# Kernel tuning notes

Measured on AMD Instinct MI355X. Metric: run time of the kernel, lower is better.

Reference implementation:

```python
import jax, jax.numpy as jnp
import numpy as np

K = 32                      # nsample (neighbors)
NPTS = [4096, 2048, 1024]   # npts // downsample_ratios [1,2,4]
CH = [(6, 64, 64), (134, 128, 128), (262, 256, 256)]  # (c_in_edge, c_mid, c_out) per EdgeConv
OUT_CH = 128
EPS = 1e-5


def setup_inputs():
    key = jax.random.key(0)
    ks = iter(jax.random.split(key, 64))
    d = {"pcd": jax.random.normal(next(ks), (8, 4096, 3), dtype=jnp.float32)}
    for li, (cin, cmid, cout) in enumerate(CH, start=1):
        d[f"W{li}a"] = jax.random.normal(next(ks), (cmid, cin), dtype=jnp.float32) * 0.05
        d[f"b{li}a"] = jax.random.normal(next(ks), (cmid,), dtype=jnp.float32) * 0.01
        d[f"g{li}a"] = jnp.ones((cmid,), dtype=jnp.float32)
        d[f"be{li}a"] = jnp.zeros((cmid,), dtype=jnp.float32)
        d[f"W{li}b"] = jax.random.normal(next(ks), (cout, cmid), dtype=jnp.float32) * 0.05
        d[f"b{li}b"] = jax.random.normal(next(ks), (cout,), dtype=jnp.float32) * 0.01
        d[f"g{li}b"] = jnp.ones((cout,), dtype=jnp.float32)
        d[f"be{li}b"] = jnp.zeros((cout,), dtype=jnp.float32)
    d["fcW"] = jax.random.normal(next(ks), (OUT_CH, CH[-1][2]), dtype=jnp.float32) * 0.05
    d["fcb"] = jnp.zeros((OUT_CH,), dtype=jnp.float32)
    return d


def _knn_idx(q, p, k):
    # q: [B,m,3] queries, p: [B,n,3] points -> [B,m,k] nearest-neighbor indices
    d = (jnp.sum(q * q, -1)[:, :, None] + jnp.sum(p * p, -1)[:, None, :]
         - 2.0 * jnp.einsum('bmd,bnd->bmn', q, p))
    _, idx = jax.lax.top_k(-d, k)
    return idx


def _bn(x, g, b):
    # training-mode BatchNorm2d over [B,C,m,k], biased variance (torch behavior)
    mu = jnp.mean(x, axis=(0, 2, 3), keepdims=True)
    var = jnp.mean((x - mu) ** 2, axis=(0, 2, 3), keepdims=True)
    return (x - mu) * jax.lax.rsqrt(var + EPS) * g[None, :, None, None] + b[None, :, None, None]


def _edge_conv(xyz, feat, npoints, params):
    # xyz: [B,n,3], feat: [B,C,n] or None. Range sampling = first npoints points.
    W1, b1, g1, be1, W2, b2, g2, be2 = params
    new_xyz = xyz[:, :npoints]
    # use_xyz=True: concat features (as [B,n,C]) with xyz
    f = xyz if feat is None else jnp.concatenate([jnp.transpose(feat, (0, 2, 1)), xyz], -1)
    new_f = f[:, :npoints]                       # [B,m,D]
    idx = _knn_idx(new_xyz, xyz, K)              # [B,m,K]
    knn_f = jax.vmap(lambda a, i: a[i])(f, idx)  # [B,m,K,D] gather
    tiled = jnp.broadcast_to(new_f[:, :, None, :], knn_f.shape)
    e = jnp.concatenate([knn_f - tiled, tiled], -1)  # [B,m,K,2D] edge features
    h = jnp.einsum('bmkc,oc->bomk', e, W1) + b1[None, :, None, None]
    h = jax.nn.relu(_bn(h, g1, be1))
    h = jnp.einsum('bcmk,oc->bomk', h, W2) + b2[None, :, None, None]
    h = jax.nn.relu(_bn(h, g2, be2))
    return new_xyz, jnp.max(h, axis=-1)          # max-pool over K -> [B,C,m]


def reference(pcd, W1a, b1a, g1a, be1a, W1b, b1b, g1b, be1b,
              W2a, b2a, g2a, be2a, W2b, b2b, g2b, be2b,
              W3a, b3a, g3a, be3a, W3b, b3b, g3b, be3b, fcW, fcb):
    xyz = pcd[..., :3]
    feat = None  # pcd has only xyz channels
    layer_params = [
        (W1a, b1a, g1a, be1a, W1b, b1b, g1b, be1b),
        (W2a, b2a, g2a, be2a, W2b, b2b, g2b, be2b),
        (W3a, b3a, g3a, be3a, W3b, b3b, g3b, be3b),
    ]
    for npoints, p in zip(NPTS, layer_params):
        xyz, feat = _edge_conv(xyz, feat, npoints, p)
    out_feat = jnp.einsum('bcn,oc->bon', feat, fcW) + fcb[None, :, None]
    # Range sampling: idx chain of aranges composes to arange(NPTS[-1])
    idx = jnp.broadcast_to(jnp.arange(NPTS[-1]), (pcd.shape[0], NPTS[-1]))
    return xyz, out_feat, idx, feat
```

## Files before the change

kernel.cpp:

```cpp
#include <hip/hip_runtime.h>
#include <hip/hip_bf16.h>

#define B8 8
#define KNN 32
typedef unsigned short u16;
typedef unsigned int u32;
typedef unsigned long long u64;

typedef __attribute__((ext_vector_type(8))) _Float16 half8;
typedef __attribute__((ext_vector_type(4))) float f32x4;

static __device__ __forceinline__ u16 f2h_u(float f) {
  _Float16 h = (_Float16)f; u16 u; __builtin_memcpy(&u, &h, 2); return u;
}

static __device__ __forceinline__ u64 enc_key(float d, int id) {
  u32 u = __float_as_uint(d);
  u = (d >= 0.f) ? (u | 0x80000000u) : ~u;
  return ((u64)u << 32) | (u32)id;
}
static __device__ __forceinline__ float dec_val(u64 k) {
  u32 u = (u32)(k >> 32);
  u = (u & 0x80000000u) ? (u & 0x7fffffffu) : ~u;
  return __uint_as_float(u);
}

static __device__ __forceinline__ u64 rank64(u64 mk, int lane, u64* slk, u64* outk, float& tau) {
  slk[lane] = mk;
  int r = 0;
#pragma unroll 16
  for (int j = 0; j < 64; ++j) r += (slk[j] < mk) ? 1 : 0;
  outk[r] = mk;
  u64 res = outk[lane];
  tau = dec_val(outk[31]);
  return res;
}

__global__ __launch_bounds__(256) void knn_kernel(const float* __restrict__ pcd,
                                                  int N, int M, int* __restrict__ idxout) {
  __shared__ float4 pts[1024];
  __shared__ u64 bufk[4][32];
  __shared__ u64 slk[4][64];
  __shared__ u64 outk[4][64];
  const int t = threadIdx.x;
  const int lane = t & 63, w = t >> 6;
  const int b = blockIdx.y;
  const int m = blockIdx.x * 4 + w;
  const float* base = pcd + (size_t)b * 4096 * 3;
  const float qx = base[m*3], qy = base[m*3+1], qz = base[m*3+2];
  const float ax = -2.f*qx, ay = -2.f*qy, az = -2.f*qz;

  u64 heldk;
  float tau;
  int cnt = 0;

  for (int i = t; i < 1024; i += 256) {
    const float* p = base + (size_t)i * 3;
    float x = p[0], y = p[1], z = p[2];
    pts[i] = make_float4(x, y, z, x*x + y*y + z*z);
  }
  __syncthreads();

  {
    float4 p = pts[lane];
    float r0 = fmaf(ax, p.x, fmaf(ay, p.y, fmaf(az, p.z, p.w)));
    heldk = rank64(enc_key(r0, lane), lane, slk[w], outk[w], tau);
  }

  for (int n0 = 0; n0 < N; n0 += 1024) {
    if (n0) {
      __syncthreads();
      for (int i = t; i < 1024; i += 256) {
        const float* p = base + (size_t)(n0 + i) * 3;
        float x = p[0], y = p[1], z = p[2];
        pts[i] = make_float4(x, y, z, x*x + y*y + z*z);
      }
      __syncthreads();
    }
    for (int c = 0; c < 1024; c += 256) {
      float4 p0 = pts[c + lane];
      float4 p1 = pts[c + 64 + lane];
      float4 p2 = pts[c + 128 + lane];
      float4 p3 = pts[c + 192 + lane];
      float r[4];
      r[0] = fmaf(ax, p0.x, fmaf(ay, p0.y, fmaf(az, p0.z, p0.w)));
      r[1] = fmaf(ax, p1.x, fmaf(ay, p1.y, fmaf(az, p1.z, p1.w)));
      r[2] = fmaf(ax, p2.x, fmaf(ay, p2.y, fmaf(az, p2.z, p2.w)));
      r[3] = fmaf(ax, p3.x, fmaf(ay, p3.y, fmaf(az, p3.z, p3.w)));
      if (n0 == 0 && c == 0) r[0] = 3.4e38f;
      float rmn = fminf(fminf(r[0], r[1]), fminf(r[2], r[3]));
      if (!__any(rmn < tau)) continue;
#pragma unroll
      for (int j = 0; j < 4; ++j) {
        float rr = r[j];
        if (!__any(rr < tau)) continue;
        int gid = n0 + c + j * 64 + lane;
        bool pass = rr < tau;
        while (__any(pass)) {
          u64 mk_ = __ballot(pass);
          int before = __popcll(mk_ & ((1ull << lane) - 1ull));
          int total  = __popcll(mk_);
          int room = 32 - cnt;
          if (pass && before < room) {
            bufk[w][cnt + before] = enc_key(rr, gid);
            pass = false;
          }
          if (total >= room) {
            u64 mk = (lane < 32) ? heldk : bufk[w][lane - 32];
            heldk = rank64(mk, lane, slk[w], outk[w], tau);
            cnt = 0;
            pass = pass && (rr < tau);
          } else {
            cnt += total;
          }
        }
      }
    }
  }
  if (cnt > 0) {
    int bl = lane - 32;
    u64 mk = (lane < 32) ? heldk
             : ((bl < cnt) ? bufk[w][bl]
                           : ((0xFFFFFFFFull << 32) | (0xFFFFFF00u | (u32)lane)));
    heldk = rank64(mk, lane, slk[w], outk[w], tau);
  }
  if (lane < KNN) idxout[((size_t)b * M + m) * KNN + lane] = (int)(u32)(heldk & 0xFFFFFFFFu);
}

__global__ void prep_all(
    const float* __restrict__ W1a, const float* __restrict__ W1b,
    const float* __restrict__ W2a, const float* __restrict__ W2b,
    const float* __restrict__ W3a, const float* __restrict__ W3b,
    float* __restrict__ RED,
    float* __restrict__ WAT1, float* __restrict__ WBT1, u16* __restrict__ WBH1,
    float* __restrict__ WBT2, u16* __restrict__ WAH2, u16* __restrict__ WBH2,
    float* __restrict__ WBT3, u16* __restrict__ WAH3, u16* __restrict__ WBH3)
{
  int i0 = blockIdx.x * 256 + threadIdx.x;
  int NT = gridDim.x * 256;
  for (int i = i0; i < 8192; i += NT) RED[i] = 0.f;
  for (int i = i0; i < 256; i += NT) {
    int c = i >> 6, o = i & 63;
    float w1 = (c < 3) ? W1a[o*6 + c] : 0.f;
    float w2 = (c < 3) ? W1a[o*6 + 3 + c] : 0.f;
    WAT1[i] = w1; WBT1[i] = w2 - w1;
  }
  for (int i = i0; i < 4096; i += NT) WBH1[i] = f2h_u(W1b[i]);
  for (int i = i0; i < 68*128; i += NT) {
    int c = i >> 7, o = i & 127;
    float w1 = 0.f, w2 = 0.f;
    if (c < 67) { w1 = W2a[o*134 + c]; w2 = W2a[o*134 + 67 + c]; }
    WBT2[i] = w2 - w1;
  }
  for (int i = i0; i < 128*128; i += NT) {
    int o = i >> 7, k = i & 127;
    WAH2[i] = (k < 67) ? f2h_u(W2a[o*134 + k]) : (u16)0;
  }
  for (int i = i0; i < 16384; i += NT) WBH2[i] = f2h_u(W2b[i]);
  for (int i = i0; i < 132*256; i += NT) {
    int c = i >> 8, o = i & 255;
    float w1 = 0.f, w2 = 0.f;
    if (c < 131) { w1 = W3a[o*262 + c]; w2 = W3a[o*262 + 131 + c]; }
    WBT3[i] = w2 - w1;
  }
  for (int i = i0; i < 256*192; i += NT) {
    int o = i / 192, k = i - o * 192;
    WAH3[i] = (k < 131) ? f2h_u(W3a[o*262 + k]) : (u16)0;
  }
  for (int i = i0; i < 65536; i += NT) WBH3[i] = f2h_u(W3b[i]);
}

template<int C2, int CM, int MODE>
__global__ __launch_bounds__(256) void conv_a_gemm(
    const float* __restrict__ F, size_t fbstride,
    const int* __restrict__ idx,
    const float* __restrict__ Wt,
    const float* __restrict__ bias,
    const float* __restrict__ T,
    float* __restrict__ Tout,
    float* __restrict__ red_s, float* __restrict__ red_q,
    int M)
{
  constexpr int KP = (C2 + 3) & ~3;
  constexpr int KC = (KP <= 68) ? KP : 44;
  __shared__ float At[64][KC];
  __shared__ float Wts[KC][64];
  __shared__ int ji[64];
  __shared__ float sred[4][64];
  __shared__ float qred[4][64];
  const int t = threadIdx.x;
  const int rt = blockIdx.x, ot = blockIdx.y, b = blockIdx.z;
  const int R0 = rt * 64, oc0 = ot * 64;
  const float* Fb = F + (size_t)b * fbstride;

  if (t < 64) {
    int gr = R0 + t;
    ji[t] = (MODE == 0) ? gr : idx[((size_t)b * M + (gr >> 5)) * KNN + (gr & 31)];
  }

  const int cg = t & 15, rg = t >> 4;
  const int r0 = rg * 4, c0 = cg * 4;
  float acc[4][4];
  if (MODE == 0) {
#pragma unroll
    for (int j = 0; j < 4; ++j) {
      float bv = bias[oc0 + c0 + j];
#pragma unroll
      for (int i = 0; i < 4; ++i) acc[i][j] = bv;
    }
  } else {
#pragma unroll
    for (int i = 0; i < 4; ++i) {
      const float* tp = T + ((size_t)b * M + (size_t)((R0 + r0 + i) >> 5)) * CM + oc0 + c0;
      acc[i][0] = tp[0]; acc[i][1] = tp[1]; acc[i][2] = tp[2]; acc[i][3] = tp[3];
    }
  }
  __syncthreads();

  for (int k0 = 0; k0 < KP; k0 += KC) {
    if (k0) __syncthreads();
    for (int i = t; i < KC * 64; i += 256) {
      int c = i >> 6, o = i & 63;
      Wts[c][o] = Wt[(size_t)(k0 + c) * CM + oc0 + o];
    }
    if constexpr (C2 == 3) {
      for (int i = t; i < 64 * 4; i += 256) {
        int r = i >> 2, c = i & 3;
        At[r][c] = (c < 3) ? Fb[(size_t)ji[r] * 3 + c] : 0.f;
      }
    } else {
      constexpr int C4 = KC / 4;
      for (int i = t; i < 64 * C4; i += 256) {
        int r = i / C4, c4 = i - r * C4;
        *(float4*)&At[r][c4 * 4] = *(const float4*)&Fb[(size_t)ji[r] * KP + k0 + c4 * 4];
      }
    }
    __syncthreads();

#pragma unroll 4
    for (int k = 0; k < KC; ++k) {
      const float4 w4 = *(const float4*)&Wts[k][c0];
      float a0 = At[r0][k], a1 = At[r0+1][k], a2 = At[r0+2][k], a3 = At[r0+3][k];
      acc[0][0]=fmaf(a0,w4.x,acc[0][0]); acc[0][1]=fmaf(a0,w4.y,acc[0][1]);
      acc[0][2]=fmaf(a0,w4.z,acc[0][2]); acc[0][3]=fmaf(a0,w4.w,acc[0][3]);
      acc[1][0]=fmaf(a1,w4.x,acc[1][0]); acc[1][1]=fmaf(a1,w4.y,acc[1][1]);
      acc[1][2]=fmaf(a1,w4.z,acc[1][2]); acc[1][3]=fmaf(a1,w4.w,acc[1][3]);
      acc[2][0]=fmaf(a2,w4.x,acc[2][0]); acc[2][1]=fmaf(a2,w4.y,acc[2][1]);
      acc[2][2]=fmaf(a2,w4.z,acc[2][2]); acc[2][3]=fmaf(a2,w4.w,acc[2][3]);
      acc[3][0]=fmaf(a3,w4.x,acc[3][0]); acc[3][1]=fmaf(a3,w4.y,acc[3][1]);
      acc[3][2]=fmaf(a3,w4.z,acc[3][2]); acc[3][3]=fmaf(a3,w4.w,acc[3][3]);
    }
  }

  if (MODE == 0) {
    float* op = Tout + ((size_t)b * M + R0) * (size_t)CM + oc0;
#pragma unroll
    for (int i = 0; i < 4; ++i) {
      float* p = op + (size_t)(r0 + i) * CM + c0;
      p[0]=acc[i][0]; p[1]=acc[i][1]; p[2]=acc[i][2]; p[3]=acc[i][3];
    }
  } else {
    float cs[4], cq_[4];
#pragma unroll
    for (int j = 0; j < 4; ++j) {
      float s = acc[0][j] + acc[1][j] + acc[2][j] + acc[3][j];
      float q = acc[0][j]*acc[0][j] + acc[1][j]*acc[1][j] + acc[2][j]*acc[2][j] + acc[3][j]*acc[3][j];
      s += __shfl_xor(s, 16); q += __shfl_xor(q, 16);
      s += __shfl_xor(s, 32); q += __shfl_xor(q, 32);
      cs[j] = s; cq_[j] = q;
    }
    const int wv = t >> 6;
    if ((t & 48) == 0) {
#pragma unroll
      for (int j = 0; j < 4; ++j) { sred[wv][c0 + j] = cs[j]; qred[wv][c0 + j] = cq_[j]; }
    }
    __syncthreads();
    if (t < 64) {
      float s = sred[0][t] + sred[1][t] + sred[2][t] + sred[3][t];
      float q = qred[0][t] + qred[1][t] + qred[2][t] + qred[3][t];
      int shdw = (rt & 15) * 256;
      atomicAdd(&red_s[shdw + t], s);
      atomicAdd(&red_q[shdw + t], q);
    }
  }
}

__global__ __launch_bounds__(256) void l1_convb(
    const float* __restrict__ pcd,
    const int* __restrict__ idx,
    const float* __restrict__ WAT,
    const float* __restrict__ T,
    const u16* __restrict__ Wbh,
    const float* __restrict__ bb,
    const float* __restrict__ sc1, const float* __restrict__ sh1,
    float* __restrict__ red_s, float* __restrict__ red_q,
    float* __restrict__ hmax)
{
  __shared__ u16 Alds[64][72];
  __shared__ u16 Wlds[64][72];
  __shared__ float xyzs[64][4];
  __shared__ float was[3][64];
  __shared__ float scs[64], shs[64];
  __shared__ int ji[64];
  const int t = threadIdx.x;
  const int lane = t & 63, w = t >> 6;
  const int wr = w >> 1, wc = w & 1;
  const int cl = lane & 15, rq = lane >> 4;
  const int rt = blockIdx.x, b = blockIdx.y;
  const int R0 = rt * 64;
  const float* pb = pcd + (size_t)b * 12288;

  if (t < 64) ji[t] = idx[((size_t)b * 4096 + ((R0 + t) >> 5)) * KNN + ((R0 + t) & 31)];
  if (t < 192) was[t / 64][t & 63] = WAT[t];
  if (t >= 192) { int c = t - 192; scs[c] = sc1[c]; shs[c] = sh1[c]; }
  if (t >= 192) {  }
  for (int i = t; i < 64 * 8; i += 256) {
    int o = i >> 3, seg = i & 7;
    *(float4*)&Wlds[o][seg * 8] = *(const float4*)&Wbh[(size_t)o * 64 + seg * 8];
  }
  __syncthreads();
  if (t < 64) {
    const float* p = pb + (size_t)ji[t] * 3;
    xyzs[t][0] = p[0]; xyzs[t][1] = p[1]; xyzs[t][2] = p[2]; xyzs[t][3] = 0.f;
  }
  if (t < 64) { scs[t] = sc1[t]; shs[t] = sh1[t]; }
  __syncthreads();

  for (int i = t; i < 64 * 8; i += 256) {
    int r = i >> 3, seg = i & 7;
    float px = xyzs[r][0], py = xyzs[r][1], pz = xyzs[r][2];
    const float* Tm = T + ((size_t)b * 4096 + (size_t)((R0 + r) >> 5)) * 64;
    half8 ov;
#pragma unroll
    for (int j2 = 0; j2 < 8; ++j2) {
      int c = seg * 8 + j2;
      float h = Tm[c];
      h = fmaf(px, was[0][c], h);
      h = fmaf(py, was[1][c], h);
      h = fmaf(pz, was[2][c], h);
      ov[j2] = (_Float16)fmaxf(0.f, fmaf(h, scs[c], shs[c]));
    }
    *(half8*)&Alds[r][seg * 8] = ov;
  }
  __syncthreads();

  f32x4 acc[2][2];
#pragma unroll
  for (int fr = 0; fr < 2; ++fr)
#pragma unroll
    for (int fc = 0; fc < 2; ++fc) {
      float bv = bb[wc * 32 + fc * 16 + cl];
#pragma unroll
      for (int r = 0; r < 4; ++r) acc[fr][fc][r] = bv;
    }

#pragma unroll
  for (int kk = 0; kk < 2; ++kk) {
    half8 af[2], bf[2];
#pragma unroll
    for (int fr = 0; fr < 2; ++fr)
      af[fr] = *(const half8*)&Alds[wr*32 + fr*16 + cl][kk*32 + rq*8];
#pragma unroll
    for (int fc = 0; fc < 2; ++fc)
      bf[fc] = *(const half8*)&Wlds[wc*32 + fc*16 + cl][kk*32 + rq*8];
#pragma unroll
    for (int fr = 0; fr < 2; ++fr)
#pragma unroll
      for (int fc = 0; fc < 2; ++fc)
        acc[fr][fc] = __builtin_amdgcn_mfma_f32_16x16x32_f16(af[fr], bf[fc], acc[fr][fc], 0, 0, 0);
  }

#pragma unroll
  for (int fc = 0; fc < 2; ++fc) {
    float s = 0.f, q = 0.f, mx = -3.4e38f;
#pragma unroll
    for (int fr = 0; fr < 2; ++fr)
#pragma unroll
      for (int r = 0; r < 4; ++r) {
        float v = acc[fr][fc][r];
        s += v; q += v * v; mx = fmaxf(mx, v);
      }
    s += __shfl_xor(s, 16); q += __shfl_xor(q, 16); mx = fmaxf(mx, __shfl_xor(mx, 16));
    s += __shfl_xor(s, 32); q += __shfl_xor(q, 32); mx = fmaxf(mx, __shfl_xor(mx, 32));
    if (rq == 0) {
      int col = wc * 32 + fc * 16 + cl;
      int shdw = (rt & 15) * 256;
      atomicAdd(&red_s[shdw + col], s);
      atomicAdd(&red_q[shdw + col], q);
      hmax[((size_t)b * 4096 + (size_t)(rt * 2 + wr)) * 64 + col] = mx;
    }
  }
}

template<int CM, int KPAD>
__global__ __launch_bounds__(256) void conv_a_mfma(
    const float* __restrict__ F, int fstride, size_t fbstride,
    const int* __restrict__ idx,
    const u16* __restrict__ Wh,
    const float* __restrict__ T,
    u16* __restrict__ Hout,
    float* __restrict__ red_s, float* __restrict__ red_q,
    int M)
{
  constexpr int FC = CM / 32;
  __shared__ u16 Alds[64][72];
  __shared__ u16 Wlds[CM][72];
  __shared__ int ji[64];
  const int t = threadIdx.x;
  const int lane = t & 63, w = t >> 6;
  const int wr = w >> 1, wc = w & 1;
  const int cl = lane & 15, rq = lane >> 4;
  const int rt = blockIdx.x, b = blockIdx.y;
  const int R0 = rt * 64;
  const float* Fb = F + (size_t)b * fbstride;

  if (t < 64) ji[t] = idx[((size_t)b * M + ((R0 + t) >> 5)) * KNN + ((R0 + t) & 31)];

  f32x4 acc[2][FC];
#pragma unroll
  for (int fr = 0; fr < 2; ++fr)
#pragma unroll
    for (int fc = 0; fc < FC; ++fc) {
      int col = wc * (CM/2) + fc * 16 + cl;
#pragma unroll
      for (int r = 0; r < 4; ++r) {
        int row = R0 + wr*32 + fr*16 + rq*4 + r;
        acc[fr][fc][r] = T[((size_t)b * M + (row >> 5)) * CM + col];
      }
    }
  __syncthreads();

  for (int k0 = 0; k0 < KPAD; k0 += 64) {
    if (k0) __syncthreads();
    for (int i = t; i < 64 * 16; i += 256) {
      int r = i >> 4, seg = i & 15;
      int k = k0 + seg * 4;
      ushort4 s = {0,0,0,0};
      if (k < fstride) {
        float4 v = *(const float4*)&Fb[(size_t)ji[r] * fstride + k];
        s.x = f2h_u(v.x); s.y = f2h_u(v.y); s.z = f2h_u(v.z); s.w = f2h_u(v.w);
      }
      *(ushort4*)&Alds[r][seg * 4] = s;
    }
    for (int i = t; i < CM * 8; i += 256) {
      int o = i >> 3, seg = i & 7;
      *(float4*)&Wlds[o][seg * 8] = *(const float4*)&Wh[(size_t)o * KPAD + k0 + seg * 8];
    }
    __syncthreads();

#pragma unroll
    for (int kk = 0; kk < 2; ++kk) {
      half8 af[2], bf[FC];
#pragma unroll
      for (int fr = 0; fr < 2; ++fr)
        af[fr] = *(const half8*)&Alds[wr*32 + fr*16 + cl][kk*32 + rq*8];
#pragma unroll
      for (int fc = 0; fc < FC; ++fc)
        bf[fc] = *(const half8*)&Wlds[wc*(CM/2) + fc*16 + cl][kk*32 + rq*8];
#pragma unroll
      for (int fr = 0; fr < 2; ++fr)
#pragma unroll
        for (int fc = 0; fc < FC; ++fc)
          acc[fr][fc] = __builtin_amdgcn_mfma_f32_16x16x32_f16(af[fr], bf[fc], acc[fr][fc], 0, 0, 0);
    }
  }

  u16* Hb = Hout + ((size_t)b * (size_t)M * KNN + R0) * CM;
#pragma unroll
  for (int fr = 0; fr < 2; ++fr)
#pragma unroll
    for (int fc = 0; fc < FC; ++fc) {
      int col = wc*(CM/2) + fc*16 + cl;
#pragma unroll
      for (int r = 0; r < 4; ++r) {
        int row = wr*32 + fr*16 + rq*4 + r;
        Hb[(size_t)row * CM + col] = f2h_u(acc[fr][fc][r]);
      }
    }

#pragma unroll
  for (int fc = 0; fc < FC; ++fc) {
    float s = 0.f, q = 0.f;
#pragma unroll
    for (int fr = 0; fr < 2; ++fr)
#pragma unroll
      for (int r = 0; r < 4; ++r) {
        float v = acc[fr][fc][r];
        s += v; q += v * v;
      }
    s += __shfl_xor(s, 16); q += __shfl_xor(q, 16);
    s += __shfl_xor(s, 32); q += __shfl_xor(q, 32);
    if (rq == 0) {
      int col = wc*(CM/2) + fc*16 + cl;
      int shdw = (rt & 15) * 256;
      atomicAdd(&red_s[shdw + col], s);
      atomicAdd(&red_q[shdw + col], q);
    }
  }
}

template<int CM>
__global__ __launch_bounds__(256) void conv_b_fused(
    const u16* __restrict__ H,
    const u16* __restrict__ Wh,
    const float* __restrict__ bb,
    const float* __restrict__ sc1, const float* __restrict__ sh1,
    float* __restrict__ red_s, float* __restrict__ red_q,
    float* __restrict__ hmax,
    int Mrows)
{
  constexpr int FC = CM / 32;
  __shared__ u16 Alds[64][72];
  __shared__ u16 Wlds[CM][72];
  __shared__ float scs[CM], shs[CM];
  const int t = threadIdx.x;
  const int lane = t & 63, w = t >> 6;
  const int wr = w >> 1, wc = w & 1;
  const int cl = lane & 15, rq = lane >> 4;
  const int rt = blockIdx.x, b = blockIdx.y;
  const u16* Hb = H + ((size_t)b * Mrows + (size_t)rt * 64) * CM;

  for (int i = t; i < CM; i += 256) { scs[i] = sc1[i]; shs[i] = sh1[i]; }

  f32x4 acc[2][FC];
#pragma unroll
  for (int fr = 0; fr < 2; ++fr)
#pragma unroll
    for (int fc = 0; fc < FC; ++fc) {
      float bv = bb[wc * (CM/2) + fc * 16 + cl];
#pragma unroll
      for (int r = 0; r < 4; ++r) acc[fr][fc][r] = bv;
    }
  __syncthreads();

  for (int k0 = 0; k0 < CM; k0 += 64) {
    if (k0) __syncthreads();
    for (int i = t; i < 64 * 8; i += 256) {
      int r = i >> 3, seg = i & 7;
      half8 hv = *(const half8*)&Hb[(size_t)r * CM + k0 + seg * 8];
      half8 ov;
#pragma unroll
      for (int j = 0; j < 8; ++j) {
        int c = k0 + seg * 8 + j;
        float v = fmaxf(0.f, fmaf((float)hv[j], scs[c], shs[c]));
        ov[j] = (_Float16)v;
      }
      *(half8*)&Alds[r][seg * 8] = ov;
    }
    for (int i = t; i < CM * 8; i += 256) {
      int o = i >> 3, seg = i & 7;
      *(float4*)&Wlds[o][seg * 8] = *(const float4*)&Wh[(size_t)o * CM + k0 + seg * 8];
    }
    __syncthreads();

#pragma unroll
    for (int kk = 0; kk < 2; ++kk) {
      half8 af[2], bf[FC];
#pragma unroll
      for (int fr = 0; fr < 2; ++fr)
        af[fr] = *(const half8*)&Alds[wr*32 + fr*16 + cl][kk*32 + rq*8];
#pragma unroll
      for (int fc = 0; fc < FC; ++fc)
        bf[fc] = *(const half8*)&Wlds[wc*(CM/2) + fc*16 + cl][kk*32 + rq*8];
#pragma unroll
      for (int fr = 0; fr < 2; ++fr)
#pragma unroll
        for (int fc = 0; fc < FC; ++fc)
          acc[fr][fc] = __builtin_amdgcn_mfma_f32_16x16x32_f16(af[fr], bf[fc], acc[fr][fc], 0, 0, 0);
    }
  }

#pragma unroll
  for (int fc = 0; fc < FC; ++fc) {
    float s = 0.f, q = 0.f, mx = -3.4e38f;
#pragma unroll
    for (int fr = 0; fr < 2; ++fr)
#pragma unroll
      for (int r = 0; r < 4; ++r) {
        float v = acc[fr][fc][r];
        s += v; q += v * v; mx = fmaxf(mx, v);
      }
    s += __shfl_xor(s, 16); q += __shfl_xor(q, 16); mx = fmaxf(mx, __shfl_xor(mx, 16));
    s += __shfl_xor(s, 32); q += __shfl_xor(q, 32); mx = fmaxf(mx, __shfl_xor(mx, 32));
    if (rq == 0) {
      int col = wc*(CM/2) + fc*16 + cl;
      int shdw = (rt & 15) * 256;
      atomicAdd(&red_s[shdw + col], s);
      atomicAdd(&red_q[shdw + col], q);
      hmax[((size_t)b * (Mrows >> 5) + (size_t)(rt * 2 + wr)) * CM + col] = mx;
    }
  }
}

__global__ void bn_finalize(float* __restrict__ red_s, float* __restrict__ red_q,
                            const float* __restrict__ g, const float* __restrict__ be,
                            float* __restrict__ sc, float* __restrict__ sh,
                            int cm, float invcnt) {
  int o = threadIdx.x;
  if (o < cm) {
    float s = 0.f, q = 0.f;
    for (int i = 0; i < 16; ++i) { s += red_s[i * 256 + o]; q += red_q[i * 256 + o]; }
    float mu  = s * invcnt;
    float var = fmaxf(q * invcnt - mu * mu, 0.f);
    float scv = g[o] * rsqrtf(var + 1e-5f);
    sc[o] = scv;
    sh[o] = fmaf(-mu, scv, be[o]);
  }
  __syncthreads();
  for (int i = threadIdx.x; i < 16 * 256; i += 256) { red_s[i] = 0.f; red_q[i] = 0.f; }
}

__global__ __launch_bounds__(256) void bnrelu_fb(const float* __restrict__ hm,
    const float* __restrict__ sc2, const float* __restrict__ sh2,
    float* __restrict__ fout, int CM, int fostride, size_t fobstride, int M) {
  int i = blockIdx.x * 256 + threadIdx.x;
  int cq = CM >> 2;
  int total = B8 * M * cq;
  if (i >= total) return;
  int c4 = i % cq; int r = i / cq;
  int b = r / M, m = r - b * M;
  float4 v = *(const float4*)&hm[((size_t)b * M + m) * CM + c4 * 4];
  int c = c4 * 4;
  float4 o;
  o.x = fmaxf(0.f, fmaf(v.x, sc2[c],   sh2[c]));
  o.y = fmaxf(0.f, fmaf(v.y, sc2[c+1], sh2[c+1]));
  o.z = fmaxf(0.f, fmaf(v.z, sc2[c+2], sh2[c+2]));
  o.w = fmaxf(0.f, fmaf(v.w, sc2[c+3], sh2[c+3]));
  *(float4*)&fout[(size_t)b * fobstride + (size_t)m * fostride + c] = o;
}

__global__ void append_xyz(const float* __restrict__ pcd, float* __restrict__ fbuf,
                           int nrows, int stride, int coff) {
  int i = blockIdx.x * 256 + threadIdx.x;
  if (i < B8 * nrows) {
    int b = i / nrows, n = i - b * nrows;
    const float* p = pcd + ((size_t)b * 4096 + n) * 3;
    float* dd = fbuf + ((size_t)b * nrows + n) * stride + coff;
    dd[0] = p[0]; dd[1] = p[1]; dd[2] = p[2]; dd[3] = 0.f;
  }
}

__global__ __launch_bounds__(256) void fc_out(const float* __restrict__ f4,
                                              const float* __restrict__ fcW, const float* __restrict__ fcb,
                                              float* __restrict__ out1, float* __restrict__ out3) {
  __shared__ float tile[32 * 257];
  const int t = threadIdx.x, b = blockIdx.x, n0 = blockIdx.y * 32;
  for (int i = t; i < 32 * 256; i += 256) {
    int n = i >> 8, c = i & 255;
    tile[n * 257 + c] = f4[((size_t)b * 1024 + n0 + n) * 256 + c];
  }
  __syncthreads();
  const int n = t & 31, og = t >> 5;
#pragma unroll
  for (int ci = 0; ci < 32; ++ci) {
    int c = og * 32 + ci;
    out3[((size_t)b * 256 + c) * 1024 + n0 + n] = tile[n * 257 + c];
  }
#pragma unroll
  for (int oi = 0; oi < 16; ++oi) {
    int o = og * 16 + oi;
    float acc = fcb[o];
    const float* w = fcW + (size_t)o * 256;
#pragma unroll 4
    for (int c = 0; c < 256; ++c) acc = fmaf(tile[n * 257 + c], w[c], acc);
    out1[((size_t)b * 128 + o) * 1024 + n0 + n] = acc;
  }
}

__global__ void out_xyz_idx(const float* __restrict__ pcd, float* __restrict__ out0,
                            float* __restrict__ out2) {
  int i = blockIdx.x * 256 + threadIdx.x;
  if (i < B8 * 1024) {
    int b = i >> 10, n = i & 1023;
    const float* p = pcd + ((size_t)b * 4096 + n) * 3;
    float* o = out0 + (size_t)i * 3;
    o[0] = p[0]; o[1] = p[1]; o[2] = p[2];
    out2[i] = (float)n;
  }
}

extern "C" void kernel_launch(void* const* d_in, const int* in_sizes, int n_in,
                              void* d_out, int out_size, void* d_ws, size_t ws_size,
                              hipStream_t stream) {
  (void)in_sizes; (void)n_in; (void)out_size; (void)ws_size;
  const float* pcd = (const float*)d_in[0];
  const float* W1a = (const float*)d_in[1];  const float* b1a = (const float*)d_in[2];
  const float* g1a = (const float*)d_in[3];  const float* be1a= (const float*)d_in[4];
  const float* W1b = (const float*)d_in[5];  const float* b1b = (const float*)d_in[6];
  const float* g1b = (const float*)d_in[7];  const float* be1b= (const float*)d_in[8];
  const float* W2a = (const float*)d_in[9];  const float* b2a = (const float*)d_in[10];
  const float* g2a = (const float*)d_in[11]; const float* be2a= (const float*)d_in[12];
  const float* W2b = (const float*)d_in[13]; const float* b2b = (const float*)d_in[14];
  const float* g2b = (const float*)d_in[15]; const float* be2b= (const float*)d_in[16];
  const float* W3a = (const float*)d_in[17]; const float* b3a = (const float*)d_in[18];
  const float* g3a = (const float*)d_in[19]; const float* be3a= (const float*)d_in[20];
  const float* W3b = (const float*)d_in[21]; const float* b3b = (const float*)d_in[22];
  const float* g3b = (const float*)d_in[23]; const float* be3b= (const float*)d_in[24];
  const float* fcW = (const float*)d_in[25]; const float* fcb = (const float*)d_in[26];

  float* wsf = (float*)d_ws;
  float* FB2 = wsf;
  float* FB3 = FB2 + 2228224;
  float* FB4 = FB3 + 2162688;
  float* TBUF= FB4 + 2097152;
  float* RED = TBUF + 2097152;
  float* red_s = RED, *red_q = RED + 4096;
  float* SC1 = RED + 8192;  float* SH1 = SC1 + 256;
  float* SC2 = SH1 + 256;   float* SH2 = SC2 + 256;
  float* WAT1 = SH2 + 256;
  float* WBT1 = WAT1 + 256;
  float* WBT2 = WBT1 + 256;
  float* WBT3 = WBT2 + 8704;
  float* HMAX = WBT3 + 33792;
  int* IDX1 = (int*)(HMAX + 2097152);
  int* IDX2 = IDX1 + (size_t)8 * 4096 * 32;
  int* IDX3 = IDX2 + (size_t)8 * 2048 * 32;
  u16* H    = (u16*)(IDX3 + (size_t)8 * 1024 * 32);
  u16* WBH1 = H + (size_t)67108864;
  u16* WAH2 = WBH1 + 4096;
  u16* WBH2 = WAH2 + 16384;
  u16* WAH3 = WBH2 + 16384;
  u16* WBH3 = WAH3 + 49152;

  float* out0 = (float*)d_out;
  float* out1 = out0 + 24576;
  float* out2 = out1 + 1048576;
  float* out3 = out2 + 8192;

  prep_all<<<64, 256, 0, stream>>>(W1a, W1b, W2a, W2b, W3a, W3b, RED,
                                   WAT1, WBT1, WBH1, WBT2, WAH2, WBH2, WBT3, WAH3, WBH3);

  knn_kernel<<<dim3(1024, 8), 256, 0, stream>>>(pcd, 4096, 4096, IDX1);
  conv_a_gemm<3,64,0><<<dim3(64,1,8),256,0,stream>>>(pcd,(size_t)12288,nullptr,WBT1,b1a,nullptr,TBUF,nullptr,nullptr,4096);
  conv_a_gemm<3,64,1><<<dim3(2048,1,8),256,0,stream>>>(pcd,(size_t)12288,IDX1,WAT1,nullptr,TBUF,nullptr,red_s,red_q,4096);
  bn_finalize<<<1,256,0,stream>>>(red_s,red_q,g1a,be1a,SC1,SH1,64,1.f/1048576.f);
  l1_convb<<<dim3(2048,8),256,0,stream>>>(pcd,IDX1,WAT1,TBUF,WBH1,b1b,SC1,SH1,red_s,red_q,HMAX);
  bn_finalize<<<1,256,0,stream>>>(red_s,red_q,g1b,be1b,SC2,SH2,64,1.f/1048576.f);
  bnrelu_fb<<<2048,256,0,stream>>>(HMAX,SC2,SH2,FB2,64,68,(size_t)278528,4096);
  append_xyz<<<128, 256, 0, stream>>>(pcd, FB2, 4096, 68, 64);

  knn_kernel<<<dim3(512, 8), 256, 0, stream>>>(pcd, 4096, 2048, IDX2);
  conv_a_gemm<67,128,0><<<dim3(32,2,8),256,0,stream>>>(FB2,(size_t)278528,nullptr,WBT2,b2a,nullptr,TBUF,nullptr,nullptr,2048);
  conv_a_mfma<128,128><<<dim3(1024,8),256,0,stream>>>(FB2,68,(size_t)278528,IDX2,WAH2,TBUF,H,red_s,red_q,2048);
  bn_finalize<<<1,256,0,stream>>>(red_s,red_q,g2a,be2a,SC1,SH1,128,1.f/524288.f);
  conv_b_fused<128><<<dim3(1024,8),256,0,stream>>>(H,WBH2,b2b,SC1,SH1,red_s,red_q,HMAX,2048*32);
  bn_finalize<<<1,256,0,stream>>>(red_s,red_q,g2b,be2b,SC2,SH2,128,1.f/524288.f);
  bnrelu_fb<<<2048,256,0,stream>>>(HMAX,SC2,SH2,FB3,128,132,(size_t)270336,2048);
  append_xyz<<<64, 256, 0, stream>>>(pcd, FB3, 2048, 132, 128);

  knn_kernel<<<dim3(256, 8), 256, 0, stream>>>(pcd, 2048, 1024, IDX3);
  conv_a_gemm<131,256,0><<<dim3(16,4,8),256,0,stream>>>(FB3,(size_t)270336,nullptr,WBT3,b3a,nullptr,TBUF,nullptr,nullptr,1024);
  conv_a_mfma<256,192><<<dim3(512,8),256,0,stream>>>(FB3,132,(size_t)270336,IDX3,WAH3,TBUF,H,red_s,red_q,1024);
  bn_finalize<<<1,256,0,stream>>>(red_s,red_q,g3a,be3a,SC1,SH1,256,1.f/262144.f);
  conv_b_fused<256><<<dim3(512,8),256,0,stream>>>(H,WBH3,b3b,SC1,SH1,red_s,red_q,HMAX,1024*32);
  bn_finalize<<<1,256,0,stream>>>(red_s,red_q,g3b,be3b,SC2,SH2,256,1.f/262144.f);
  bnrelu_fb<<<2048,256,0,stream>>>(HMAX,SC2,SH2,FB4,256,256,(size_t)262144,1024);

  fc_out<<<dim3(8, 32), 256, 0, stream>>>(FB4, fcW, fcb, out1, out3);
  out_xyz_idx<<<32, 256, 0, stream>>>(pcd, out0, out2);
}
```

Before: 872.7 us.

## Store conv_a intermediate in FP8 and widen KNN blocks to 512 threads

The conv_a_mfma output H, which was stored as fp16 per element, is now packed as four FP8 values per u32, with the four rows of an MFMA fragment sharing one word. conv_b_fused unpacks these bytes back to float before applying BN and ReLU. This halves the traffic for the large intermediate but lowers its precision, which could exceed the accuracy tolerance. Separately, the KNN kernel now uses 512-thread blocks with a 2048-point LDS tile and N as a template parameter, and a redundant load of the scale and shift values is dropped.

After: 880.5 us. No clear change (+0.9%).

```diff
diff --git a/kernel.cpp b/kernel.cpp
--- a/kernel.cpp
+++ b/kernel.cpp
@@ -36,25 +36,24 @@
   return res;
 }
 
-__global__ __launch_bounds__(256) void knn_kernel(const float* __restrict__ pcd,
-                                                  int N, int M, int* __restrict__ idxout) {
-  __shared__ float4 pts[1024];
-  __shared__ u64 bufk[4][32];
-  __shared__ u64 slk[4][64];
-  __shared__ u64 outk[4][64];
+template<int N>
+__global__ __launch_bounds__(512) void knn_kernel(const float* __restrict__ pcd,
+                                                  int M, int* __restrict__ idxout) {
+  __shared__ float4 pts[2048];
+  __shared__ u64 slk[8][64];
+  __shared__ u64 outk[8][64];
+  __shared__ u64 bufk[8][32];
   const int t = threadIdx.x;
   const int lane = t & 63, w = t >> 6;
   const int b = blockIdx.y;
-  const int m = blockIdx.x * 4 + w;
+  const int m = blockIdx.x * 8 + w;
   const float* base = pcd + (size_t)b * 4096 * 3;
   const float qx = base[m*3], qy = base[m*3+1], qz = base[m*3+2];
   const float ax = -2.f*qx, ay = -2.f*qy, az = -2.f*qz;
 
-  u64 heldk;
-  float tau;
-  int cnt = 0;
-
-  for (int i = t; i < 1024; i += 256) {
+  u64 heldk; float tau; int cnt = 0;
+
+  for (int i = t; i < 2048; i += 512) {
     const float* p = base + (size_t)i * 3;
     float x = p[0], y = p[1], z = p[2];
     pts[i] = make_float4(x, y, z, x*x + y*y + z*z);
@@ -67,17 +66,17 @@
     heldk = rank64(enc_key(r0, lane), lane, slk[w], outk[w], tau);
   }
 
-  for (int n0 = 0; n0 < N; n0 += 1024) {
-    if (n0) {
+  for (int t0 = 0; t0 < N; t0 += 2048) {
+    if (t0) {
       __syncthreads();
-      for (int i = t; i < 1024; i += 256) {
-        const float* p = base + (size_t)(n0 + i) * 3;
+      for (int i = t; i < 2048; i += 512) {
+        const float* p = base + (size_t)(t0 + i) * 3;
         float x = p[0], y = p[1], z = p[2];
         pts[i] = make_float4(x, y, z, x*x + y*y + z*z);
       }
       __syncthreads();
     }
-    for (int c = 0; c < 1024; c += 256) {
+    for (int c = 0; c < 2048; c += 256) {
       float4 p0 = pts[c + lane];
       float4 p1 = pts[c + 64 + lane];
       float4 p2 = pts[c + 128 + lane];
@@ -87,14 +86,14 @@
       r[1] = fmaf(ax, p1.x, fmaf(ay, p1.y, fmaf(az, p1.z, p1.w)));
       r[2] = fmaf(ax, p2.x, fmaf(ay, p2.y, fmaf(az, p2.z, p2.w)));
       r[3] = fmaf(ax, p3.x, fmaf(ay, p3.y, fmaf(az, p3.z, p3.w)));
-      if (n0 == 0 && c == 0) r[0] = 3.4e38f;
+      if (t0 == 0 && c == 0) r[0] = 3.4e38f;
       float rmn = fminf(fminf(r[0], r[1]), fminf(r[2], r[3]));
       if (!__any(rmn < tau)) continue;
 #pragma unroll
       for (int j = 0; j < 4; ++j) {
         float rr = r[j];
         if (!__any(rr < tau)) continue;
-        int gid = n0 + c + j * 64 + lane;
+        int gid = t0 + c + j * 64 + lane;
         bool pass = rr < tau;
         while (__any(pass)) {
           u64 mk_ = __ballot(pass);
@@ -312,8 +311,6 @@
 
   if (t < 64) ji[t] = idx[((size_t)b * 4096 + ((R0 + t) >> 5)) * KNN + ((R0 + t) & 31)];
   if (t < 192) was[t / 64][t & 63] = WAT[t];
-  if (t >= 192) { int c = t - 192; scs[c] = sc1[c]; shs[c] = sh1[c]; }
-  if (t >= 192) {  }
   for (int i = t; i < 64 * 8; i += 256) {
     int o = i >> 3, seg = i & 7;
     *(float4*)&Wlds[o][seg * 8] = *(const float4*)&Wbh[(size_t)o * 64 + seg * 8];
@@ -398,7 +395,7 @@
     const int* __restrict__ idx,
     const u16* __restrict__ Wh,
     const float* __restrict__ T,
-    u16* __restrict__ Hout,
+    u32* __restrict__ H32,
     float* __restrict__ red_s, float* __restrict__ red_q,
     int M)
 {
@@ -465,17 +462,15 @@
     }
   }
 
-  u16* Hb = Hout + ((size_t)b * (size_t)M * KNN + R0) * CM;
+  u32* Hb4 = H32 + ((size_t)b * ((size_t)M * KNN / 4) + (size_t)(R0 >> 2)) * CM;
 #pragma unroll
   for (int fr = 0; fr < 2; ++fr)
 #pragma unroll
     for (int fc = 0; fc < FC; ++fc) {
       int col = wc*(CM/2) + fc*16 + cl;
-#pragma unroll
-      for (int r = 0; r < 4; ++r) {
-        int row = wr*32 + fr*16 + rq*4 + r;
-        Hb[(size_t)row * CM + col] = f2h_u(acc[fr][fc][r]);
-      }
+      u32 v = __builtin_amdgcn_cvt_pk_fp8_f32(acc[fr][fc][0], acc[fr][fc][1], 0, false);
+      v = __builtin_amdgcn_cvt_pk_fp8_f32(acc[fr][fc][2], acc[fr][fc][3], v, true);
+      Hb4[(size_t)(wr*8 + fr*4 + rq) * CM + col] = v;
     }
 
 #pragma unroll
@@ -501,7 +496,7 @@
 
 template<int CM>
 __global__ __launch_bounds__(256) void conv_b_fused(
-    const u16* __restrict__ H,
+    const u32* __restrict__ H32,
     const u16* __restrict__ Wh,
     const float* __restrict__ bb,
     const float* __restrict__ sc1, const float* __restrict__ sh1,
@@ -518,7 +513,7 @@
   const int wr = w >> 1, wc = w & 1;
   const int cl = lane & 15, rq = lane >> 4;
   const int rt = blockIdx.x, b = blockIdx.y;
-  const u16* Hb = H + ((size_t)b * Mrows + (size_t)rt * 64) * CM;
+  const u32* Hb4 = H32 + ((size_t)b * ((size_t)Mrows / 4) + (size_t)(rt * 16)) * CM;
 
   for (int i = t; i < CM; i += 256) { scs[i] = sc1[i]; shs[i] = sh1[i]; }
 
@@ -537,12 +532,14 @@
     if (k0) __syncthreads();
     for (int i = t; i < 64 * 8; i += 256) {
       int r = i >> 3, seg = i & 7;
-      half8 hv = *(const half8*)&Hb[(size_t)r * CM + k0 + seg * 8];
+      int rg = r >> 2, sh8 = (r & 3) * 8;
+      const u32* hp = Hb4 + (size_t)rg * CM + k0 + seg * 8;
       half8 ov;
 #pragma unroll
       for (int j = 0; j < 8; ++j) {
+        float v = __builtin_amdgcn_cvt_f32_fp8((hp[j] >> sh8) & 0xffu, 0);
         int c = k0 + seg * 8 + j;
-        float v = fmaxf(0.f, fmaf((float)hv[j], scs[c], shs[c]));
+        v = fmaxf(0.f, fmaf(v, scs[c], shs[c]));
         ov[j] = (_Float16)v;
       }
       *(half8*)&Alds[r][seg * 8] = ov;
@@ -715,8 +712,8 @@
   int* IDX1 = (int*)(HMAX + 2097152);
   int* IDX2 = IDX1 + (size_t)8 * 4096 * 32;
   int* IDX3 = IDX2 + (size_t)8 * 2048 * 32;
-  u16* H    = (u16*)(IDX3 + (size_t)8 * 1024 * 32);
-  u16* WBH1 = H + (size_t)67108864;
+  u32* H32  = (u32*)(IDX3 + (size_t)8 * 1024 * 32);
+  u16* WBH1 = (u16*)(H32 + 16777216);
   u16* WAH2 = WBH1 + 4096;
   u16* WBH2 = WAH2 + 16384;
   u16* WAH3 = WBH2 + 16384;
@@ -730,7 +727,7 @@
   prep_all<<<64, 256, 0, stream>>>(W1a, W1b, W2a, W2b, W3a, W3b, RED,
                                    WAT1, WBT1, WBH1, WBT2, WAH2, WBH2, WBT3, WAH3, WBH3);
 
-  knn_kernel<<<dim3(1024, 8), 256, 0, stream>>>(pcd, 4096, 4096, IDX1);
+  knn_kernel<4096><<<dim3(512, 8), 512, 0, stream>>>(pcd, 4096, IDX1);
   conv_a_gemm<3,64,0><<<dim3(64,1,8),256,0,stream>>>(pcd,(size_t)12288,nullptr,WBT1,b1a,nullptr,TBUF,nullptr,nullptr,4096);
   conv_a_gemm<3,64,1><<<dim3(2048,1,8),256,0,stream>>>(pcd,(size_t)12288,IDX1,WAT1,nullptr,TBUF,nullptr,red_s,red_q,4096);
   bn_finalize<<<1,256,0,stream>>>(red_s,red_q,g1a,be1a,SC1,SH1,64,1.f/1048576.f);
@@ -739,20 +736,20 @@
   bnrelu_fb<<<2048,256,0,stream>>>(HMAX,SC2,SH2,FB2,64,68,(size_t)278528,4096);
   append_xyz<<<128, 256, 0, stream>>>(pcd, FB2, 4096, 68, 64);
 
-  knn_kernel<<<dim3(512, 8), 256, 0, stream>>>(pcd, 4096, 2048, IDX2);
+  knn_kernel<4096><<<dim3(256, 8), 512, 0, stream>>>(pcd, 2048, IDX2);
   conv_a_gemm<67,128,0><<<dim3(32,2,8),256,0,stream>>>(FB2,(size_t)278528,nullptr,WBT2,b2a,nullptr,TBUF,nullptr,nullptr,2048);
-  conv_a_mfma<128,128><<<dim3(1024,8),256,0,stream>>>(FB2,68,(size_t)278528,IDX2,WAH2,TBUF,H,red_s,red_q,2048);
+  conv_a_mfma<128,128><<<dim3(1024,8),256,0,stream>>>(FB2,68,(size_t)278528,IDX2,WAH2,TBUF,H32,red_s,red_q,2048);
   bn_finalize<<<1,256,0,stream>>>(red_s,red_q,g2a,be2a,SC1,SH1,128,1.f/524288.f);
-  conv_b_fused<128><<<dim3(1024,8),256,0,stream>>>(H,WBH2,b2b,SC1,SH1,red_s,red_q,HMAX,2048*32);
+  conv_b_fused<128><<<dim3(1024,8),256,0,stream>>>(H32,WBH2,b2b,SC1,SH1,red_s,red_q,HMAX,2048*32);
   bn_finalize<<<1,256,0,stream>>>(red_s,red_q,g2b,be2b,SC2,SH2,128,1.f/524288.f);
   bnrelu_fb<<<2048,256,0,stream>>>(HMAX,SC2,SH2,FB3,128,132,(size_t)270336,2048);
   append_xyz<<<64, 256, 0, stream>>>(pcd, FB3, 2048, 132, 128);
 
-  knn_kernel<<<dim3(256, 8), 256, 0, stream>>>(pcd, 2048, 1024, IDX3);
+  knn_kernel<2048><<<dim3(128, 8), 512, 0, stream>>>(pcd, 1024, IDX3);
   conv_a_gemm<131,256,0><<<dim3(16,4,8),256,0,stream>>>(FB3,(size_t)270336,nullptr,WBT3,b3a,nullptr,TBUF,nullptr,nullptr,1024);
-  conv_a_mfma<256,192><<<dim3(512,8),256,0,stream>>>(FB3,132,(size_t)270336,IDX3,WAH3,TBUF,H,red_s,red_q,1024);
+  conv_a_mfma<256,192><<<dim3(512,8),256,0,stream>>>(FB3,132,(size_t)270336,IDX3,WAH3,TBUF,H32,red_s,red_q,1024);
   bn_finalize<<<1,256,0,stream>>>(red_s,red_q,g3a,be3a,SC1,SH1,256,1.f/262144.f);
-  conv_b_fused<256><<<dim3(512,8),256,0,stream>>>(H,WBH3,b3b,SC1,SH1,red_s,red_q,HMAX,1024*32);
+  conv_b_fused<256><<<dim3(512,8),256,0,stream>>>(H32,WBH3,b3b,SC1,SH1,red_s,red_q,HMAX,1024*32);
   bn_finalize<<<1,256,0,stream>>>(red_s,red_q,g3b,be3b,SC2,SH2,256,1.f/262144.f);
   bnrelu_fb<<<2048,256,0,stream>>>(HMAX,SC2,SH2,FB4,256,256,(size_t)262144,1024);
 
```
